# Kernel tuning notes

Hardware: AMD Instinct MI355X
Metric: run time of the kernel (lower is better)

The kernel has to match this reference:

```python
import jax, jax.numpy as jnp
import numpy as np

D_MODEL = 1024
N_HEADS = 16
HEAD_DIM = D_MODEL // N_HEADS  # 64
SEQ = 2048
BATCH = 1
LOG2_E = 1.44269504


def _rope_freqs(seq, head_dim, theta=10000.0):
    inv_freq = 1.0 / (theta ** (np.arange(0, head_dim, 2, dtype=np.float32) / head_dim))
    angles = np.outer(np.arange(seq, dtype=np.float32), inv_freq)  # [seq, head_dim/2]
    return jnp.asarray(np.cos(angles)), jnp.asarray(np.sin(angles))


def setup_inputs() -> dict:
    key = jax.random.key(0)
    ks = jax.random.split(key, 5)
    scale = 1.0 / np.sqrt(D_MODEL)
    x = jax.random.normal(ks[0], (BATCH, SEQ, D_MODEL), dtype=jnp.float32)
    wq = jax.random.normal(ks[1], (D_MODEL, D_MODEL), dtype=jnp.float32) * scale
    wk = jax.random.normal(ks[2], (D_MODEL, D_MODEL), dtype=jnp.float32) * scale
    wv = jax.random.normal(ks[3], (D_MODEL, D_MODEL), dtype=jnp.float32) * scale
    wo = jax.random.normal(ks[4], (D_MODEL, D_MODEL), dtype=jnp.float32) * scale
    freqs_cos, freqs_sin = _rope_freqs(SEQ, HEAD_DIM)
    return {"x": x, "wq": wq, "wk": wk, "wv": wv, "wo": wo,
            "freqs_cos": freqs_cos, "freqs_sin": freqs_sin}


def _apply_rope(x, cos, sin):
    # x: [b, s, h, d]; cos/sin: [s, d/2]. Complex multiply on (even, odd) pairs.
    xr = x.reshape(x.shape[:-1] + (HEAD_DIM // 2, 2))
    x0, x1 = xr[..., 0], xr[..., 1]
    c = cos[None, :, None, :]
    s = sin[None, :, None, :]
    o0 = x0 * c - x1 * s
    o1 = x0 * s + x1 * c
    return jnp.stack([o0, o1], axis=-1).reshape(x.shape)


def reference(x, wq, wk, wv, wo, freqs_cos, freqs_sin):
    b, s, _ = x.shape
    # Linear(bias=False): y = x @ W.T (torch convention)
    q = (x @ wq.T).reshape(b, s, N_HEADS, HEAD_DIM)
    k = (x @ wk.T).reshape(b, s, N_HEADS, HEAD_DIM)
    v = (x @ wv.T).reshape(b, s, N_HEADS, HEAD_DIM)
    q = _apply_rope(q, freqs_cos, freqs_sin)
    k = _apply_rope(k, freqs_cos, freqs_sin)
    # -> [b, h, s, d]
    q = q.transpose(0, 2, 1, 3)
    k = k.transpose(0, 2, 1, 3)
    v = v.transpose(0, 2, 1, 3)
    scores = jnp.einsum('bhqd,bhkd->bhqk', q, k) * (HEAD_DIM ** -0.5)
    log_w = jax.nn.log_softmax(scores, axis=-1)
    attn_weights = jnp.exp(log_w)
    entropy = (-jnp.sum(attn_weights * log_w, axis=-1) * LOG2_E).transpose(0, 2, 1)  # [b, s, h]
    out = jnp.einsum('bhqk,bhkd->bhqd', attn_weights, v)
    out = out.transpose(0, 2, 1, 3).reshape(b, s, -1)
    return out @ wo.T, attn_weights, entropy
```

## Files before the change

kernel.cpp:

```cpp
#include <hip/hip_runtime.h>


typedef __attribute__((ext_vector_type(8))) unsigned short u16x8;
typedef __attribute__((ext_vector_type(8))) short s16x8;
typedef __attribute__((ext_vector_type(4))) float f32x4;

__device__ __forceinline__ unsigned short f2b(float f) {
  unsigned int u = __float_as_uint(f);
  return (unsigned short)((u + 0x7fffu + ((u >> 16) & 1u)) >> 16);
}

__device__ __forceinline__ int swz64(int row, int col)  { return row * 64  + (col ^ ((row & 7) << 3)); }
__device__ __forceinline__ int swz128(int row, int col) { return row * 128 + (col ^ ((row & 7) << 3)); }

__device__ __forceinline__ void gload16(const void* g, void* l) {
  __builtin_amdgcn_global_load_lds((const __attribute__((address_space(1))) void*)g,
                                   (__attribute__((address_space(3))) void*)l, 16, 0, 0);
}

__global__ __launch_bounds__(256) void cast_all_kernel(const float* __restrict__ x,
    const float* __restrict__ wq, const float* __restrict__ wk, const float* __restrict__ wv,
    const float* __restrict__ wo, unsigned short* __restrict__ xbf,
    unsigned short* __restrict__ wbf, unsigned short* __restrict__ wobf) {
  int i = blockIdx.x * 256 + threadIdx.x;
  const float* src;
  unsigned short* dst;
  if (i < 262144) {
    src = x + (size_t)i * 8; dst = xbf + (size_t)i * 8;
  } else {
    int j = i - 262144;
    int seg = j >> 17, rem = j & 131071;
    if (seg == 3)      { src = wo + (size_t)rem * 8; dst = wobf + (size_t)rem * 8; }
    else if (seg == 0) { src = wq + (size_t)rem * 8; dst = wbf + (size_t)rem * 8; }
    else if (seg == 1) { src = wk + (size_t)rem * 8; dst = wbf + 1048576 + (size_t)rem * 8; }
    else               { src = wv + (size_t)rem * 8; dst = wbf + 2097152 + (size_t)rem * 8; }
  }
  u16x8 o;
#pragma unroll
  for (int j = 0; j < 8; ++j) o[j] = f2b(src[j]);
  *(u16x8*)dst = o;
}

__global__ __launch_bounds__(256) void gemm_qkv_kernel(const unsigned short* __restrict__ A,
    const unsigned short* __restrict__ B, const float* __restrict__ fcos,
    const float* __restrict__ fsin, unsigned short* __restrict__ qbf,
    unsigned short* __restrict__ kbf, unsigned short* __restrict__ vt) {
  const int K = 1024;
  int bx = blockIdx.x;
  int m0 = blockIdx.y * 128;
  int n0 = bx * 64;
  int tid = threadIdx.x, lane = tid & 63, w = tid >> 6;
  int cl = lane & 15, hw = lane >> 4;
  int wr = w * 32;

  __shared__ unsigned short smem[24576];
  unsigned short* As = smem;
  unsigned short* Bs = smem + 16384;

  int lrow8 = lane >> 3;
  int loct = (lane & 7) ^ lrow8;
  const unsigned short* gA = A + (size_t)(m0 + wr + lrow8) * K + loct * 8;
  const unsigned short* gB = B + (size_t)(n0 + w * 16 + lrow8) * K + loct * 8;

  auto stage = [&](int buf, int k0) {
    unsigned short* as = As + buf * 8192;
    unsigned short* bs = Bs + buf * 4096;
#pragma unroll
    for (int j = 0; j < 4; ++j)
      gload16(gA + (size_t)(8 * j) * K + k0, as + (wr + 8 * j) * 64);
#pragma unroll
    for (int j = 0; j < 2; ++j)
      gload16(gB + (size_t)(8 * j) * K + k0, bs + (w * 16 + 8 * j) * 64);
  };

  f32x4 acc[2][4];
#pragma unroll
  for (int i = 0; i < 2; ++i)
#pragma unroll
    for (int j = 0; j < 4; ++j) acc[i][j] = (f32x4){0.f, 0.f, 0.f, 0.f};

  stage(0, 0);
  __syncthreads();
  for (int t = 0; t < 16; ++t) {
    if (t < 15) stage((t + 1) & 1, (t + 1) * 64);
    const unsigned short* as = As + (t & 1) * 8192;
    const unsigned short* bs = Bs + (t & 1) * 4096;
#pragma unroll
    for (int kk = 0; kk < 2; ++kk) {
      s16x8 af[2], bf[4];
#pragma unroll
      for (int i = 0; i < 2; ++i)
        af[i] = *(const s16x8*)(as + swz64(wr + i * 16 + cl, kk * 32 + hw * 8));
#pragma unroll
      for (int j = 0; j < 4; ++j)
        bf[j] = *(const s16x8*)(bs + swz64(j * 16 + cl, kk * 32 + hw * 8));
#pragma unroll
      for (int i = 0; i < 2; ++i)
#pragma unroll
        for (int j = 0; j < 4; ++j)
          acc[i][j] = __builtin_amdgcn_mfma_f32_16x16x32_bf16(af[i], bf[j], acc[i][j], 0, 0, 0);
    }
    __syncthreads();
  }

  int sel = bx >> 4;
  if (sel < 2) {
    float* cosl = (float*)smem;
    float* sinl = cosl + 128 * 33;
    for (int t = tid; t < 4096; t += 256) {
      cosl[(t >> 5) * 33 + (t & 31)] = fcos[(size_t)m0 * 32 + t];
      sinl[(t >> 5) * 33 + (t & 31)] = fsin[(size_t)m0 * 32 + t];
    }
    __syncthreads();
    unsigned short* dst = sel ? kbf : qbf;
    int cbase = (bx & 15) * 64;
#pragma unroll
    for (int i = 0; i < 2; ++i)
#pragma unroll
      for (int j = 0; j < 4; ++j)
#pragma unroll
        for (int r = 0; r < 4; ++r) {
          int rl = wr + i * 16 + hw * 4 + r;
          int c = cbase + j * 16 + cl;
          float v = acc[i][j][r];
          float pvv = __shfl_xor(v, 1);
          int pair = (c & 63) >> 1;
          float cc = cosl[rl * 33 + pair];
          float ss = sinl[rl * 33 + pair];
          float o = (c & 1) ? (pvv * ss + v * cc) : (v * cc - pvv * ss);
          dst[(size_t)(m0 + rl) * 1024 + c] = f2b(o);
        }
  } else {
    unsigned short* T = smem;
#pragma unroll
    for (int i = 0; i < 2; ++i)
#pragma unroll
      for (int j = 0; j < 4; ++j) {
        int dl = j * 16 + cl;
        int sl = wr + i * 16 + hw * 4;
        ushort4 pk;
        pk.x = f2b(acc[i][j][0]); pk.y = f2b(acc[i][j][1]);
        pk.z = f2b(acc[i][j][2]); pk.w = f2b(acc[i][j][3]);
        *(ushort4*)(T + swz128(dl, sl)) = pk;
      }
    __syncthreads();
    int dbase = (bx & 15) * 64;
    for (int t = tid; t < 1024; t += 256) {
      int dl = t >> 4, sl = (t & 15) << 3;
      u16x8 val = *(const u16x8*)(T + swz128(dl, sl));
      *(u16x8*)(vt + (size_t)(dbase + dl) * 2048 + m0 + sl) = val;
    }
  }
}

__global__ __launch_bounds__(256) void gemm_out_kernel(const unsigned short* __restrict__ A,
    const unsigned short* __restrict__ B, float* __restrict__ C) {
  const int K = 1024, N = 1024;
  int n0 = blockIdx.x * 64, m0 = blockIdx.y * 64;
  int tid = threadIdx.x, lane = tid & 63, w = tid >> 6;
  int cl = lane & 15, hw = lane >> 4;

  __shared__ unsigned short As[2 * 64 * 64], Bs[2 * 64 * 64];

  int lrow8 = lane >> 3;
  int loct = (lane & 7) ^ lrow8;
  const unsigned short* gA = A + (size_t)(m0 + w * 16 + lrow8) * K + loct * 8;
  const unsigned short* gB = B + (size_t)(n0 + w * 16 + lrow8) * K + loct * 8;

  auto stage = [&](int buf, int k0) {
#pragma unroll
    for (int j = 0; j < 2; ++j) {
      gload16(gA + (size_t)(8 * j) * K + k0, As + buf * 4096 + (w * 16 + 8 * j) * 64);
      gload16(gB + (size_t)(8 * j) * K + k0, Bs + buf * 4096 + (w * 16 + 8 * j) * 64);
    }
  };

  f32x4 acc[4];
#pragma unroll
  for (int j = 0; j < 4; ++j) acc[j] = (f32x4){0.f, 0.f, 0.f, 0.f};

  stage(0, 0);
  __syncthreads();
  for (int t = 0; t < 16; ++t) {
    if (t < 15) stage((t + 1) & 1, (t + 1) * 64);
    const unsigned short* as = As + (t & 1) * 4096;
    const unsigned short* bs = Bs + (t & 1) * 4096;
#pragma unroll
    for (int kk = 0; kk < 2; ++kk) {
      s16x8 af = *(const s16x8*)(as + swz64(w * 16 + cl, kk * 32 + hw * 8));
#pragma unroll
      for (int j = 0; j < 4; ++j) {
        s16x8 bf = *(const s16x8*)(bs + swz64(j * 16 + cl, kk * 32 + hw * 8));
        acc[j] = __builtin_amdgcn_mfma_f32_16x16x32_bf16(af, bf, acc[j], 0, 0, 0);
      }
    }
    __syncthreads();
  }
#pragma unroll
  for (int j = 0; j < 4; ++j)
#pragma unroll
    for (int r = 0; r < 4; ++r)
      C[(size_t)(m0 + w * 16 + hw * 4 + r) * N + n0 + j * 16 + cl] = acc[j][r];
}

__global__ __launch_bounds__(256) void attn_kernel(const unsigned short* __restrict__ Qbf,
                                                   const unsigned short* __restrict__ Kbf,
                                                   const unsigned short* __restrict__ Vt,
                                                   float* __restrict__ attnw,
                                                   float* __restrict__ ent,
                                                   unsigned short* __restrict__ attno) {
  const float SCL = 0.18033688f;
  int h = blockIdx.x, qb = blockIdx.y;
  int q0 = qb * 64;
  int tid = threadIdx.x, lane = tid & 63, w = tid >> 6;
  int qr = w * 16, cl = lane & 15, hw = lane >> 4;

  __shared__ unsigned short smem[40960];
  unsigned short* Ps = smem;

  int lrow8 = lane >> 3;
  int koct = (lane & 7) ^ lrow8;
  int vrow4 = lane >> 4;
  const unsigned short* gKb = Kbf + h * 64 + koct * 8;
  const unsigned short* gVbase = Vt + (size_t)(h * 64 + w * 16 + vrow4) * 2048;

  auto stageK1 = [&](int buf, int kc) {
    unsigned short* dst = smem + 8192 + buf * 16384;
#pragma unroll
    for (int j = 0; j < 8; ++j)
      gload16(gKb + (size_t)(kc + w * 64 + 8 * j + lrow8) * 1024, dst + (w * 64 + 8 * j) * 64);
  };
  auto stageK2 = [&](int buf, int kc) {
    unsigned short* dst = smem + 8192 + buf * 8192;
#pragma unroll
    for (int j = 0; j < 4; ++j)
      gload16(gKb + (size_t)(kc + w * 32 + 8 * j + lrow8) * 1024, dst + (w * 32 + 8 * j) * 64);
  };
  auto stageV = [&](int buf, int kc) {
    unsigned short* dst = smem + 24576 + buf * 8192;
#pragma unroll
    for (int j = 0; j < 4; ++j) {
      int voct = (lane & 15) ^ ((4 * j + vrow4) & 7);
      gload16(gVbase + (size_t)(4 * j) * 2048 + kc + voct * 8, dst + (w * 16 + 4 * j) * 128);
    }
  };

  const unsigned short* qrow = Qbf + (size_t)(q0 + qr + cl) * 1024 + h * 64 + hw * 8;
  s16x8 qa0 = *(const s16x8*)(qrow);
  s16x8 qa1 = *(const s16x8*)(qrow + 32);

  float l_acc = 0.f, es_acc = 0.f;

  stageK1(0, 0);
  __syncthreads();
  for (int t = 0; t < 8; ++t) {
    if (t < 7) stageK1((t + 1) & 1, (t + 1) * 256);
    const unsigned short* ks = smem + 8192 + (t & 1) * 16384;
#pragma unroll
    for (int j = 0; j < 16; ++j) {
      f32x4 c = (f32x4){0.f, 0.f, 0.f, 0.f};
      s16x8 kf0 = *(const s16x8*)(ks + swz64(j * 16 + cl, hw * 8));
      s16x8 kf1 = *(const s16x8*)(ks + swz64(j * 16 + cl, 32 + hw * 8));
      c = __builtin_amdgcn_mfma_f32_16x16x32_bf16(kf0, qa0, c, 0, 0, 0);
      c = __builtin_amdgcn_mfma_f32_16x16x32_bf16(kf1, qa1, c, 0, 0, 0);
#pragma unroll
      for (int r = 0; r < 4; ++r) {
        float c2 = c[r] * SCL;
        float e = exp2f(c2);
        l_acc += e;
        es_acc = fmaf(e, c2, es_acc);
      }
    }
    __syncthreads();
  }

  stageK2(0, 0);
  stageV(0, 0);

  l_acc += __shfl_xor(l_acc, 16);  l_acc += __shfl_xor(l_acc, 32);
  es_acc += __shfl_xor(es_acc, 16); es_acc += __shfl_xor(es_acc, 32);
  float linv = 1.f / l_acc;
  if (lane < 16)
    ent[(size_t)(q0 + qr + lane) * 16 + h] = log2f(l_acc) - es_acc * linv;

  f32x4 pv[4];
#pragma unroll
  for (int dj = 0; dj < 4; ++dj) pv[dj] = (f32x4){0.f, 0.f, 0.f, 0.f};

  float* awrow = attnw + ((size_t)h << 22) + (size_t)(q0 + qr + cl) * 2048;

  __syncthreads();
  for (int t = 0; t < 16; ++t) {
    if (t < 15) { stageK2((t + 1) & 1, (t + 1) * 128); stageV((t + 1) & 1, (t + 1) * 128); }
    int kc = t * 128;
    const unsigned short* ks = smem + 8192 + (t & 1) * 8192;
    const unsigned short* vs = smem + 24576 + (t & 1) * 8192;
#pragma unroll
    for (int j = 0; j < 8; ++j) {
      f32x4 c = (f32x4){0.f, 0.f, 0.f, 0.f};
      s16x8 kf0 = *(const s16x8*)(ks + swz64(j * 16 + cl, hw * 8));
      s16x8 kf1 = *(const s16x8*)(ks + swz64(j * 16 + cl, 32 + hw * 8));
      c = __builtin_amdgcn_mfma_f32_16x16x32_bf16(kf0, qa0, c, 0, 0, 0);
      c = __builtin_amdgcn_mfma_f32_16x16x32_bf16(kf1, qa1, c, 0, 0, 0);
      f32x4 p;
#pragma unroll
      for (int r = 0; r < 4; ++r) p[r] = exp2f(c[r] * SCL) * linv;
      *(f32x4*)(awrow + kc + j * 16 + hw * 4) = p;
      ushort4 pk;
      pk.x = f2b(p[0]); pk.y = f2b(p[1]); pk.z = f2b(p[2]); pk.w = f2b(p[3]);
      *(ushort4*)(Ps + swz128(qr + cl, j * 16 + hw * 4)) = pk;
    }
    s16x8 pa[4];
#pragma unroll
    for (int kk2 = 0; kk2 < 4; ++kk2)
      pa[kk2] = *(const s16x8*)(Ps + swz128(qr + cl, kk2 * 32 + hw * 8));
#pragma unroll
    for (int dj = 0; dj < 4; ++dj) {
      f32x4 cc = pv[dj];
#pragma unroll
      for (int kk2 = 0; kk2 < 4; ++kk2) {
        s16x8 vb = *(const s16x8*)(vs + swz128(dj * 16 + cl, kk2 * 32 + hw * 8));
        cc = __builtin_amdgcn_mfma_f32_16x16x32_bf16(pa[kk2], vb, cc, 0, 0, 0);
      }
      pv[dj] = cc;
    }
    __syncthreads();
  }

#pragma unroll
  for (int dj = 0; dj < 4; ++dj)
#pragma unroll
    for (int r = 0; r < 4; ++r) {
      int row = q0 + qr + hw * 4 + r;
      int col = h * 64 + dj * 16 + cl;
      attno[(size_t)row * 1024 + col] = f2b(pv[dj][r]);
    }
}

extern "C" void kernel_launch(void* const* d_in, const int* in_sizes, int n_in,
                              void* d_out, int out_size, void* d_ws, size_t ws_size,
                              hipStream_t stream) {
  const float* x  = (const float*)d_in[0];
  const float* wq = (const float*)d_in[1];
  const float* wk = (const float*)d_in[2];
  const float* wv = (const float*)d_in[3];
  const float* wo = (const float*)d_in[4];
  const float* fc = (const float*)d_in[5];
  const float* fs = (const float*)d_in[6];

  float* out0  = (float*)d_out;
  float* attnw = out0 + (size_t)2048 * 1024;
  float* ent   = attnw + (size_t)16 * 2048 * 2048;

  char* ws = (char*)d_ws;
  unsigned short* xbf  = (unsigned short*)(ws);
  unsigned short* wbf  = (unsigned short*)(ws + (4u  << 20));
  unsigned short* wobf = (unsigned short*)(ws + (10u << 20));
  unsigned short* qbf  = (unsigned short*)(ws + (12u << 20));
  unsigned short* kbf  = (unsigned short*)(ws + (16u << 20));
  unsigned short* vtbf = (unsigned short*)(ws + (20u << 20));
  unsigned short* aobf = (unsigned short*)(ws + (24u << 20));

  cast_all_kernel<<<3072, 256, 0, stream>>>(x, wq, wk, wv, wo, xbf, wbf, wobf);
  gemm_qkv_kernel<<<dim3(48, 16), 256, 0, stream>>>(xbf, wbf, fc, fs, qbf, kbf, vtbf);
  attn_kernel<<<dim3(16, 32), 256, 0, stream>>>(qbf, kbf, vtbf, attnw, ent, aobf);
  gemm_out_kernel<<<dim3(16, 32), 256, 0, stream>>>(aobf, wobf, out0);
}
```

Baseline: 141.6 us.

## Stage attention weights through LDS for coalesced global stores, shrink key tiles

The attention kernel now writes each fp32 probability tile into a swizzled LDS buffer and then reads it back row-wise, so the stores to the large attention-weights output become contiguous full-row writes instead of scattered 16-byte fragments. Key tiles drop from 256/128 to 128/64 keys per iteration, and the K/V staging is reorganized with an XOR swizzle on 16-byte chunks. This targets write coalescing on the dominant 256 MB output, at the cost of extra LDS traffic, more LDS usage (56 KB, which may lower occupancy) and twice as many loop iterations and barriers.

Result: slower. 148.5 us (+4.9%).

```diff
diff --git a/kernel.cpp b/kernel.cpp
--- a/kernel.cpp
+++ b/kernel.cpp
@@ -214,34 +214,32 @@
   int q0 = qb * 64;
   int tid = threadIdx.x, lane = tid & 63, w = tid >> 6;
   int qr = w * 16, cl = lane & 15, hw = lane >> 4;
-
-  __shared__ unsigned short smem[40960];
-  unsigned short* Ps = smem;
-
-  int lrow8 = lane >> 3;
-  int koct = (lane & 7) ^ lrow8;
-  int vrow4 = lane >> 4;
-  const unsigned short* gKb = Kbf + h * 64 + koct * 8;
-  const unsigned short* gVbase = Vt + (size_t)(h * 64 + w * 16 + vrow4) * 2048;
+  int l8 = lane >> 3, o8 = lane & 7;
+
+  __shared__ alignas(16) unsigned char smem[57344];
 
   auto stageK1 = [&](int buf, int kc) {
-    unsigned short* dst = smem + 8192 + buf * 16384;
-#pragma unroll
-    for (int j = 0; j < 8; ++j)
-      gload16(gKb + (size_t)(kc + w * 64 + 8 * j + lrow8) * 1024, dst + (w * 64 + 8 * j) * 64);
+    unsigned char* base = smem + 24576 + buf * 16384 + w * 1024;
+#pragma unroll
+    for (int i = 0; i < 4; ++i) {
+      int row = i * 32 + w * 8 + l8;
+      gload16(Kbf + (size_t)(kc + row) * 1024 + h * 64 + (o8 ^ (row & 7)) * 8, base + i * 4096);
+    }
   };
   auto stageK2 = [&](int buf, int kc) {
-    unsigned short* dst = smem + 8192 + buf * 8192;
-#pragma unroll
-    for (int j = 0; j < 4; ++j)
-      gload16(gKb + (size_t)(kc + w * 32 + 8 * j + lrow8) * 1024, dst + (w * 32 + 8 * j) * 64);
+    unsigned char* base = smem + 24576 + buf * 8192 + w * 1024;
+#pragma unroll
+    for (int i = 0; i < 2; ++i) {
+      int row = i * 32 + w * 8 + l8;
+      gload16(Kbf + (size_t)(kc + row) * 1024 + h * 64 + (o8 ^ (row & 7)) * 8, base + i * 4096);
+    }
   };
   auto stageV = [&](int buf, int kc) {
-    unsigned short* dst = smem + 24576 + buf * 8192;
-#pragma unroll
-    for (int j = 0; j < 4; ++j) {
-      int voct = (lane & 15) ^ ((4 * j + vrow4) & 7);
-      gload16(gVbase + (size_t)(4 * j) * 2048 + kc + voct * 8, dst + (w * 16 + 4 * j) * 128);
+    unsigned char* base = smem + 40960 + buf * 8192 + w * 1024;
+#pragma unroll
+    for (int i = 0; i < 2; ++i) {
+      int row = i * 32 + w * 8 + l8;
+      gload16(Vt + (size_t)(h * 64 + row) * 2048 + kc + (o8 ^ (row & 7)) * 8, base + i * 4096);
     }
   };
 
@@ -253,14 +251,15 @@
 
   stageK1(0, 0);
   __syncthreads();
-  for (int t = 0; t < 8; ++t) {
-    if (t < 7) stageK1((t + 1) & 1, (t + 1) * 256);
-    const unsigned short* ks = smem + 8192 + (t & 1) * 16384;
-#pragma unroll
-    for (int j = 0; j < 16; ++j) {
+  for (int t = 0; t < 16; ++t) {
+    if (t < 15) stageK1((t + 1) & 1, (t + 1) * 128);
+    const unsigned char* ks = smem + 24576 + (t & 1) * 16384;
+#pragma unroll
+    for (int j = 0; j < 8; ++j) {
+      int key = j * 16 + cl;
       f32x4 c = (f32x4){0.f, 0.f, 0.f, 0.f};
-      s16x8 kf0 = *(const s16x8*)(ks + swz64(j * 16 + cl, hw * 8));
-      s16x8 kf1 = *(const s16x8*)(ks + swz64(j * 16 + cl, 32 + hw * 8));
+      s16x8 kf0 = *(const s16x8*)(ks + key * 128 + ((hw ^ (key & 7)) * 16));
+      s16x8 kf1 = *(const s16x8*)(ks + key * 128 + (((4 + hw) ^ (key & 7)) * 16));
       c = __builtin_amdgcn_mfma_f32_16x16x32_bf16(kf0, qa0, c, 0, 0, 0);
       c = __builtin_amdgcn_mfma_f32_16x16x32_bf16(kf1, qa1, c, 0, 0, 0);
 #pragma unroll
@@ -287,39 +286,46 @@
 #pragma unroll
   for (int dj = 0; dj < 4; ++dj) pv[dj] = (f32x4){0.f, 0.f, 0.f, 0.f};
 
-  float* awrow = attnw + ((size_t)h << 22) + (size_t)(q0 + qr + cl) * 2048;
-
   __syncthreads();
-  for (int t = 0; t < 16; ++t) {
-    if (t < 15) { stageK2((t + 1) & 1, (t + 1) * 128); stageV((t + 1) & 1, (t + 1) * 128); }
-    int kc = t * 128;
-    const unsigned short* ks = smem + 8192 + (t & 1) * 8192;
-    const unsigned short* vs = smem + 24576 + (t & 1) * 8192;
-#pragma unroll
-    for (int j = 0; j < 8; ++j) {
+  for (int t = 0; t < 32; ++t) {
+    if (t < 31) { stageK2((t + 1) & 1, (t + 1) * 64); stageV((t + 1) & 1, (t + 1) * 64); }
+    int kc = t * 64;
+    const unsigned char* ks = smem + 24576 + (t & 1) * 8192;
+    const unsigned char* vs = smem + 40960 + (t & 1) * 8192;
+    int prow = qr + cl;
+#pragma unroll
+    for (int j = 0; j < 4; ++j) {
+      int key = j * 16 + cl;
       f32x4 c = (f32x4){0.f, 0.f, 0.f, 0.f};
-      s16x8 kf0 = *(const s16x8*)(ks + swz64(j * 16 + cl, hw * 8));
-      s16x8 kf1 = *(const s16x8*)(ks + swz64(j * 16 + cl, 32 + hw * 8));
+      s16x8 kf0 = *(const s16x8*)(ks + key * 128 + ((hw ^ (key & 7)) * 16));
+      s16x8 kf1 = *(const s16x8*)(ks + key * 128 + (((4 + hw) ^ (key & 7)) * 16));
       c = __builtin_amdgcn_mfma_f32_16x16x32_bf16(kf0, qa0, c, 0, 0, 0);
       c = __builtin_amdgcn_mfma_f32_16x16x32_bf16(kf1, qa1, c, 0, 0, 0);
       f32x4 p;
 #pragma unroll
       for (int r = 0; r < 4; ++r) p[r] = exp2f(c[r] * SCL) * linv;
-      *(f32x4*)(awrow + kc + j * 16 + hw * 4) = p;
+      *(f32x4*)(smem + 8192 + prow * 256 + (((j * 4 + hw) ^ (cl & 7)) * 16)) = p;
       ushort4 pk;
       pk.x = f2b(p[0]); pk.y = f2b(p[1]); pk.z = f2b(p[2]); pk.w = f2b(p[3]);
-      *(ushort4*)(Ps + swz128(qr + cl, j * 16 + hw * 4)) = pk;
-    }
-    s16x8 pa[4];
-#pragma unroll
-    for (int kk2 = 0; kk2 < 4; ++kk2)
-      pa[kk2] = *(const s16x8*)(Ps + swz128(qr + cl, kk2 * 32 + hw * 8));
+      *(ushort4*)(smem + prow * 128 + (((j * 2 + (hw >> 1)) ^ (cl & 7)) * 16) + (hw & 1) * 8) = pk;
+    }
+#pragma unroll
+    for (int i = 0; i < 4; ++i) {
+      int row = qr + i * 4 + hw;
+      f32x4 v = *(const f32x4*)(smem + 8192 + row * 256 + ((cl ^ (row & 7)) * 16));
+      *(f32x4*)(attnw + ((size_t)h << 22) + (size_t)(q0 + row) * 2048 + kc + cl * 4) = v;
+    }
+    s16x8 pa[2];
+#pragma unroll
+    for (int kk2 = 0; kk2 < 2; ++kk2)
+      pa[kk2] = *(const s16x8*)(smem + prow * 128 + (((kk2 * 4 + hw) ^ (cl & 7)) * 16));
 #pragma unroll
     for (int dj = 0; dj < 4; ++dj) {
+      int d = dj * 16 + cl;
       f32x4 cc = pv[dj];
 #pragma unroll
-      for (int kk2 = 0; kk2 < 4; ++kk2) {
-        s16x8 vb = *(const s16x8*)(vs + swz128(dj * 16 + cl, kk2 * 32 + hw * 8));
+      for (int kk2 = 0; kk2 < 2; ++kk2) {
+        s16x8 vb = *(const s16x8*)(vs + d * 128 + (((kk2 * 4 + hw) ^ (d & 7)) * 16));
         cc = __builtin_amdgcn_mfma_f32_16x16x32_bf16(pa[kk2], vb, cc, 0, 0, 0);
       }
       pv[dj] = cc;
```
